# Optimization experiments

Measured on AMD Instinct MI355X. Metric: run time of the kernel, lower is better.

Reference implementation:

```python
import jax, jax.numpy as jnp
import numpy as np

B, N, D_MAX_LEN, D_LENGTH, D_MODEL, N_CLASS = 16, 1024, 512, 256, 128, 10
SAMPLE_K = 140  # factor(20) * ceil(ln(1024)) = 20*7; also n_top u (L_Q == L_K)


def setup_inputs() -> dict:
    key = jax.random.key(0)
    ks = jax.random.split(key, 10)
    s = 0.02
    return {
        "input_embedding": jax.random.normal(ks[0], (B, N, D_MAX_LEN), jnp.float32),
        "index_sample": jax.random.randint(ks[1], (N, SAMPLE_K), 0, N),
        # weights stored [in, out] (transpose of torch Linear.weight)
        "W_lin": jax.random.normal(ks[2], (D_MAX_LEN, D_LENGTH), jnp.float32) * s,
        "b_lin": jnp.zeros((D_LENGTH,), jnp.float32),
        "W_q": jax.random.normal(ks[3], (D_LENGTH, D_MODEL), jnp.float32) * s,
        "W_k": jax.random.normal(ks[4], (D_LENGTH, D_MODEL), jnp.float32) * s,
        "W_v": jax.random.normal(ks[5], (D_LENGTH, D_MODEL), jnp.float32) * s,
        "W_add": jax.random.normal(ks[6], (D_LENGTH, D_MODEL), jnp.float32) * s,
        "b_add": jnp.zeros((D_MODEL,), jnp.float32),
        "W_final": jax.random.normal(ks[7], (D_MODEL * N, N_CLASS), jnp.float32) * s,
        "b_final": jnp.zeros((N_CLASS,), jnp.float32),
    }


def reference(input_embedding, index_sample, W_lin, b_lin, W_q, W_k, W_v,
              W_add, b_add, W_final, b_final):
    # self.linear: [B, N, d_max_len] -> [B, N, d_length]
    x = input_embedding @ W_lin + b_lin
    b, n, _ = x.shape
    # single head (h=1): [B, 1, L, D]
    Q = (x @ W_q)[:, None]
    K = (x @ W_k)[:, None]
    V = (x @ W_v)[:, None]
    d = Q.shape[-1]
    L_K = n
    n_top = index_sample.shape[1]  # u == sample_k here

    # _prob_QK: gather sampled keys per query row, score against Q
    Kg = K[:, :, index_sample, :]                      # [B,1,L_Q,S,D]
    QK_sample = jnp.einsum('bhld,bhlsd->bhls', Q, Kg)  # [B,1,L_Q,S]
    M = QK_sample.max(-1) - QK_sample.sum(-1) / L_K    # sparsity measure
    _, M_top = jax.lax.top_k(M, n_top)                 # [B,1,u]

    Qr = jnp.take_along_axis(Q, M_top[..., None], axis=2)       # [B,1,u,D]
    scores = jnp.einsum('bhud,bhkd->bhuk', Qr, K) / np.sqrt(d)  # [B,1,u,L_K]

    # _get_initial_context (mask_flag=False): mean of V broadcast over L_Q
    ctx = jnp.broadcast_to(V.mean(axis=2, keepdims=True), V.shape)  # [B,1,L_Q,D]

    # _update_context: scatter softmax(scores) @ V into selected rows
    attn = jax.nn.softmax(scores, axis=-1)
    upd = jnp.einsum('bhuk,bhkd->bhud', attn, V)  # [B,1,u,D]
    bidx = jnp.arange(b)[:, None, None]
    hidx = jnp.arange(1)[None, :, None]
    ctx = ctx.at[bidx, hidx, M_top].set(upd)

    ctx = ctx[:, 0]                    # H=1 -> [B,N,D]
    out = ctx + (x @ W_add + b_add)    # residual add (dropout: eval mode)
    out = out.reshape(b, -1) @ W_final + b_final  # [B, n_class]
    return out
```

## Files before the change

### kernel.cpp

```cpp
#include <hip/hip_runtime.h>

typedef __attribute__((ext_vector_type(8))) short short8;
typedef __attribute__((ext_vector_type(8))) unsigned short ushort8;
typedef __attribute__((ext_vector_type(4))) float f32x4;
typedef unsigned short u16;
typedef unsigned int u32;
typedef __attribute__((address_space(1))) const u32 gu32;
typedef __attribute__((address_space(3))) u32 lu32;

__device__ __forceinline__ u16 f2bf(float f){
  unsigned u = __float_as_uint(f);
  u += 0x7FFF + ((u >> 16) & 1);
  return (u16)(u >> 16);
}
__device__ __forceinline__ float bf2f(u16 h){ return __uint_as_float(((unsigned)h) << 16); }

#define BB   16
#define NN   1024
#define DML  512
#define DL   256
#define DM   128
#define NC   10
#define SK   140
#define KTOT (NN*DM)

__global__ void k_prep(const float* __restrict__ Wlin, const float* __restrict__ Wq,
                       const float* __restrict__ Wk, const float* __restrict__ Wv,
                       const float* __restrict__ Wadd,
                       u16* __restrict__ wlinT, u16* __restrict__ w4T,
                       const float* __restrict__ Wf, u16* __restrict__ wf2,
                       const int* __restrict__ idxs, u16* __restrict__ idxp){
  int blk = blockIdx.x, t = threadIdx.x;
  if (blk < 512){
    int id = blk*256 + t;
    {
      int j = id >> 9;
      int k = id & 511;
      wlinT[id] = f2bf(Wlin[k*DL + j]);
    }
    {
      int j = id >> 8;
      int k = id & 255;
      const float* src = (j < 128) ? Wq : (j < 256) ? Wk : (j < 384) ? Wv : Wadd;
      int jj = j & 127;
      w4T[id] = f2bf(src[k*DM + jj]);
    }
  } else if (blk < 1792){
    int i4 = (blk-512)*256 + t;
    float4 v = ((const float4*)Wf)[i4];
    ushort4 o; o.x=f2bf(v.x); o.y=f2bf(v.y); o.z=f2bf(v.z); o.w=f2bf(v.w);
    ((ushort4*)wf2)[i4] = o;
  } else {
    int id = (blk-1792)*256 + t;
    int l = id / 144;
    int s = id - l*144;
    idxp[id] = (s < SK) ? (u16)idxs[l*SK + s] : (u16)0xFFFF;
  }
}

__device__ __forceinline__ void stage2(const u16* __restrict__ A, const u16* __restrict__ B,
                                       int K, int m0, int n0, int kb,
                                       u16* sA, u16* sB, int tid, int wave){
  #pragma unroll
  for (int i = 0; i < 4; ++i){
    int ci  = i*256 + tid;
    int row = ci >> 3;
    int kc  = (ci & 7) ^ (row & 7);
    __builtin_amdgcn_global_load_lds((gu32*)(A + (long)(m0+row)*K + kb + kc*8),
                                     (lu32*)(sA + (i*256 + wave*64)*8), 16, 0, 0);
    __builtin_amdgcn_global_load_lds((gu32*)(B + (long)(n0+row)*K + kb + kc*8),
                                     (lu32*)(sB + (i*256 + wave*64)*8), 16, 0, 0);
  }
}
__device__ __forceinline__ void compute64(const u16* sA, const u16* sB,
                                          int lane, int wrow, int wcol, f32x4 acc[4][4]){
  #pragma unroll
  for (int kk = 0; kk < 2; ++kk){
    short8 af[4], bfr[4];
    int cb = kk*4 + (lane >> 4);
    #pragma unroll
    for (int m_=0; m_<4; ++m_){
      int row = wrow + m_*16 + (lane & 15);
      af[m_] = *(const short8*)&sA[row*64 + ((cb ^ (row & 7)) << 3)];
    }
    #pragma unroll
    for (int n_=0; n_<4; ++n_){
      int row = wcol + n_*16 + (lane & 15);
      bfr[n_] = *(const short8*)&sB[row*64 + ((cb ^ (row & 7)) << 3)];
    }
    #pragma unroll
    for (int m_=0; m_<4; ++m_)
      #pragma unroll
      for (int n_=0; n_<4; ++n_)
        acc[m_][n_] = __builtin_amdgcn_mfma_f32_16x16x32_bf16(af[m_], bfr[n_], acc[m_][n_], 0, 0, 0);
  }
}

__global__ __launch_bounds__(256) void k_gemm_x(const float* __restrict__ A, const u16* __restrict__ B,
                                                const float* __restrict__ bias, u16* __restrict__ out){
  __shared__ u16 smem[12288];
  u16* sA = smem;
  u16* sB = smem + 4096;
  const int tid  = threadIdx.x;
  const int lane = tid & 63;
  const int wave = tid >> 6;
  const int wrow = (wave >> 1) * 32;
  const int wcol = (wave & 1) * 64;
  int m0 = blockIdx.x*64, n0 = blockIdx.y*128;
  f32x4 acc[2][4];
  f32x4 z = {0.f,0.f,0.f,0.f};
  #pragma unroll
  for (int m_=0;m_<2;++m_) for (int n_=0;n_<4;++n_) acc[m_][n_] = z;

  f32x4 ra[4];
  short8 rb[4];
  const int arow = tid >> 2, aq = tid & 3;

  {
    const float* src = A + (long)(m0+arow)*DML + aq*16;
    ra[0] = ((const f32x4*)src)[0]; ra[1] = ((const f32x4*)src)[1];
    ra[2] = ((const f32x4*)src)[2]; ra[3] = ((const f32x4*)src)[3];
    #pragma unroll
    for (int i=0;i<4;++i){
      int ci = i*256 + tid, row = ci>>3, kc = ci&7;
      rb[i] = *(const short8*)(B + (long)(n0+row)*DML + kc*8);
    }
  }
  {
    short8 o0, o1;
    #pragma unroll
    for (int j=0;j<4;++j){ o0[j]=(short)f2bf(ra[0][j]); o0[4+j]=(short)f2bf(ra[1][j]);
                           o1[j]=(short)f2bf(ra[2][j]); o1[4+j]=(short)f2bf(ra[3][j]); }
    int kc0 = aq*2, kc1 = aq*2+1;
    *(short8*)&sA[arow*64 + ((kc0 ^ (arow&7))<<3)] = o0;
    *(short8*)&sA[arow*64 + ((kc1 ^ (arow&7))<<3)] = o1;
    #pragma unroll
    for (int i=0;i<4;++i){
      int ci = i*256 + tid, row = ci>>3, kc = ci&7;
      *(short8*)&sB[row*64 + ((kc ^ (row&7))<<3)] = rb[i];
    }
  }
  __syncthreads();

  for (int tt = 0; tt < 8; ++tt){
    if (tt < 7){
      int kb = (tt+1)*64;
      const float* src = A + (long)(m0+arow)*DML + kb + aq*16;
      ra[0] = ((const f32x4*)src)[0]; ra[1] = ((const f32x4*)src)[1];
      ra[2] = ((const f32x4*)src)[2]; ra[3] = ((const f32x4*)src)[3];
      #pragma unroll
      for (int i=0;i<4;++i){
        int ci = i*256 + tid, row = ci>>3, kc = ci&7;
        rb[i] = *(const short8*)(B + (long)(n0+row)*DML + kb + kc*8);
      }
    }
    #pragma unroll
    for (int kk = 0; kk < 2; ++kk){
      short8 af[2], bfr[4];
      int cb = kk*4 + (lane >> 4);
      #pragma unroll
      for (int m_=0; m_<2; ++m_){
        int row = wrow + m_*16 + (lane & 15);
        af[m_] = *(const short8*)&sA[row*64 + ((cb ^ (row & 7)) << 3)];
      }
      #pragma unroll
      for (int n_=0; n_<4; ++n_){
        int row = wcol + n_*16 + (lane & 15);
        bfr[n_] = *(const short8*)&sB[row*64 + ((cb ^ (row & 7)) << 3)];
      }
      #pragma unroll
      for (int m_=0; m_<2; ++m_)
        #pragma unroll
        for (int n_=0; n_<4; ++n_)
          acc[m_][n_] = __builtin_amdgcn_mfma_f32_16x16x32_bf16(af[m_], bfr[n_], acc[m_][n_], 0, 0, 0);
    }
    __syncthreads();
    if (tt < 7){
      short8 o0, o1;
      #pragma unroll
      for (int j=0;j<4;++j){ o0[j]=(short)f2bf(ra[0][j]); o0[4+j]=(short)f2bf(ra[1][j]);
                             o1[j]=(short)f2bf(ra[2][j]); o1[4+j]=(short)f2bf(ra[3][j]); }
      int kc0 = aq*2, kc1 = aq*2+1;
      *(short8*)&sA[arow*64 + ((kc0 ^ (arow&7))<<3)] = o0;
      *(short8*)&sA[arow*64 + ((kc1 ^ (arow&7))<<3)] = o1;
      #pragma unroll
      for (int i=0;i<4;++i){
        int ci = i*256 + tid, row = ci>>3, kc = ci&7;
        *(short8*)&sB[row*64 + ((kc ^ (row&7))<<3)] = rb[i];
      }
      __syncthreads();
    }
  }

  u16* sC = sB;
  #pragma unroll
  for (int m_=0;m_<2;++m_)
    #pragma unroll
    for (int n_=0;n_<4;++n_)
      #pragma unroll
      for (int rr=0;rr<4;++rr){
        int row = wrow + m_*16 + (lane>>4)*4 + rr;
        int col = wcol + n_*16 + (lane & 15);
        sC[row*128 + col] = f2bf(acc[m_][n_][rr] + bias[n0 + col]);
      }
  __syncthreads();
  #pragma unroll
  for (int i = 0; i < 4; ++i){
    int ci = i*256 + tid;
    int row = ci >> 4, c = ci & 15;
    *(short8*)(out + (long)(m0+row)*DL + n0 + c*8) = *(const short8*)&sC[row*128 + c*8];
  }
}

__global__ __launch_bounds__(256) void k_gemm_qkva(const u16* __restrict__ A, const u16* __restrict__ B,
                                                   const float* __restrict__ badd,
                                                   u16* __restrict__ oq, u16* __restrict__ ok,
                                                   u16* __restrict__ ov, u16* __restrict__ oa,
                                                   u16* __restrict__ vT){
  __shared__ u16 smem[17408];
  u16* sA = smem;
  u16* sB = smem + 8192;
  const int tid = threadIdx.x, lane = tid & 63, wave = tid >> 6;
  const int wrow = (wave>>1)*64, wcol = (wave&1)*64;
  f32x4 acc[4][4];
  f32x4 z = {0.f,0.f,0.f,0.f};
  #pragma unroll
  for (int m_=0;m_<4;++m_) for (int n_=0;n_<4;++n_) acc[m_][n_] = z;
  int m0 = blockIdx.x*128;
  int tn = blockIdx.y;
  int n0 = tn*128;

  #pragma unroll
  for (int t = 0; t < 4; ++t){
    stage2(A, B, DL, m0, n0, t*64, sA, sB, tid, wave);
    __syncthreads();
    compute64(sA, sB, lane, wrow, wcol, acc);
    __syncthreads();
  }

  u16* dst = (tn==0) ? oq : (tn==1) ? ok : (tn==2) ? ov : oa;
  u16* sC = smem;
  #pragma unroll
  for (int m_=0;m_<4;++m_)
    #pragma unroll
    for (int n_=0;n_<4;++n_)
      #pragma unroll
      for (int r=0;r<4;++r){
        int row = wrow + m_*16 + (lane>>4)*4 + r;
        int col = wcol + n_*16 + (lane & 15);
        float v = acc[m_][n_][r];
        if (tn == 3) v += badd[col];
        sC[row*136 + col] = f2bf(v);
      }
  __syncthreads();
  u16* db = dst + (long)m0*DM;
  #pragma unroll
  for (int i = 0; i < 8; ++i){
    int ci = i*256 + tid;
    int row = ci >> 4, c = ci & 15;
    *(short8*)(db + (long)row*DM + c*8) = *(const short8*)&sC[row*136 + c*8];
  }
  if (tn == 2){
    int b2 = m0 >> 10, l0 = m0 & 1023;
    u16* vtb = vT + (long)b2*KTOT + l0;
    #pragma unroll
    for (int i = 0; i < 8; ++i){
      int gi = i*256 + tid;
      int d = gi >> 4, mc = gi & 15;
      ushort8 o;
      #pragma unroll
      for (int j = 0; j < 8; ++j) o[j] = sC[(mc*8+j)*136 + d];
      *(ushort8*)(vtb + (long)d*NN + mc*8) = o;
    }
  }
}

__global__ __launch_bounds__(256) void k_gemm_s(const u16* __restrict__ Q, const u16* __restrict__ Km,
                                                u16* __restrict__ S, const u16* __restrict__ idxp,
                                                float* __restrict__ pmax, float* __restrict__ psum){
  __shared__ u16 smem[16384];
  u16* sA = smem;
  u16* sB = smem + 8192;
  const int tid = threadIdx.x, lane = tid & 63, wave = tid >> 6;
  const int wrow = (wave>>1)*64, wcol = (wave&1)*64;
  f32x4 acc[4][4];
  f32x4 z = {0.f,0.f,0.f,0.f};
  #pragma unroll
  for (int m_=0;m_<4;++m_) for (int n_=0;n_<4;++n_) acc[m_][n_] = z;
  int b = blockIdx.x, n0 = blockIdx.y*128, m0 = blockIdx.z*128;
  const u16* A = Q  + (long)b*NN*DM;
  const u16* B = Km + (long)b*NN*DM;

  stage2(A, B, DM, m0, n0, 0, sA, sB, tid, wave);
  __syncthreads();
  compute64(sA, sB, lane, wrow, wcol, acc);
  __syncthreads();
  stage2(A, B, DM, m0, n0, 64, sA, sB, tid, wave);
  __syncthreads();
  compute64(sA, sB, lane, wrow, wcol, acc);
  __syncthreads();

  u16* sS = smem;
  #pragma unroll
  for (int m_=0;m_<4;++m_)
    #pragma unroll
    for (int n_=0;n_<4;++n_)
      #pragma unroll
      for (int r=0;r<4;++r){
        int row = wrow + m_*16 + (lane>>4)*4 + r;
        int col = wcol + n_*16 + (lane & 15);
        sS[row*128 + col] = f2bf(acc[m_][n_][r]);
      }
  __syncthreads();

  u16* Sb = S + (long)b*NN*NN + (long)m0*NN + n0;
  #pragma unroll
  for (int i = 0; i < 8; ++i){
    int ci = i*256 + tid;
    int row = ci >> 4, c = ci & 15;
    *(short8*)(Sb + (long)row*NN + c*8) = *(const short8*)&sS[row*128 + c*8];
  }

  int l = tid >> 1, h = tid & 1;
  const u16* ip = idxp + (long)(m0+l)*144 + h*72;
  float mx = -1e30f, sm = 0.f;
  #pragma unroll
  for (int j = 0; j < 9; ++j){
    ushort8 v = *(const ushort8*)(ip + j*8);
    #pragma unroll
    for (int e = 0; e < 8; ++e){
      int d = (int)v[e] - n0;
      if ((unsigned)d < 128u){
        float s = bf2f(sS[l*128 + d]);
        mx = fmaxf(mx, s); sm += s;
      }
    }
  }
  float mo = __shfl_xor(mx, 1), so = __shfl_xor(sm, 1);
  mx = fmaxf(mx, mo); sm += so;
  if (h == 0){
    int o = (b*8 + blockIdx.y)*NN + m0 + l;
    pmax[o] = mx; psum[o] = sm;
  }
}

__global__ __launch_bounds__(256) void k_rankvm(const float* __restrict__ pmax, const float* __restrict__ psum,
                                                int* __restrict__ partial,
                                                const u16* __restrict__ V, float* __restrict__ vmean){
  int blk = blockIdx.x, t = threadIdx.x;
  if (blk < 256){
    __shared__ float Ml[1024];
    int b = blk >> 4, jc = blk & 15;
    #pragma unroll
    for (int r=0;r<4;++r){
      int i = t + r*256;
      float mx = -1e30f, sm = 0.f;
      #pragma unroll
      for (int nb=0;nb<8;++nb){
        mx = fmaxf(mx, pmax[(b*8+nb)*NN + i]);
        sm += psum[(b*8+nb)*NN + i];
      }
      Ml[i] = mx - sm * (1.0f/1024.0f);
    }
    __syncthreads();
    float mi[4];
    int cnt[4] = {0,0,0,0};
    #pragma unroll
    for (int r=0;r<4;++r) mi[r] = Ml[t + r*256];
    int j0 = jc*64;
    for (int j = 0; j < 64; ++j){
      float mj = Ml[j0 + j];
      int jg = j0 + j;
      #pragma unroll
      for (int r=0;r<4;++r){
        int i = t + r*256;
        cnt[r] += (mj > mi[r]) || (mj == mi[r] && jg < i);
      }
    }
    int* pb = partial + (b*16 + jc)*NN;
    #pragma unroll
    for (int r=0;r<4;++r) pb[t + r*256] = cnt[r];
  } else {
    __shared__ float red[16][128];
    int b = blk - 256;
    int d8 = t & 15, seg = t >> 4;
    const u16* Vb = V + (long)b*KTOT + seg*64*DM + d8*8;
    float acc[8] = {0,0,0,0,0,0,0,0};
    for (int l = 0; l < 64; ++l){
      short8 v = *(const short8*)(Vb + l*DM);
      #pragma unroll
      for (int j=0;j<8;++j) acc[j] += bf2f((u16)v[j]);
    }
    #pragma unroll
    for (int j=0;j<8;++j) red[seg][d8*8+j] = acc[j];
    __syncthreads();
    if (t < 128){
      float s = 0.f;
      #pragma unroll
      for (int g=0;g<16;++g) s += red[g][t];
      vmean[b*DM + t] = s * (1.0f/1024.0f);
    }
  }
}

__global__ __launch_bounds__(1024) void k_sel(const int* __restrict__ partial, int* __restrict__ mtop,
                                              int* __restrict__ selmap){
  int b = blockIdx.x, i = threadIdx.x;
  int cnt = 0;
  #pragma unroll
  for (int jc = 0; jc < 16; ++jc) cnt += partial[(b*16 + jc)*NN + i];
  selmap[b*NN + i] = (cnt < SK) ? cnt : -1;
  if (cnt < SK) mtop[b*SK + cnt] = i;
}

__global__ __launch_bounds__(256) void k_attn(const u16* __restrict__ S, const u16* __restrict__ vT,
                                              const int* __restrict__ mtop, float* __restrict__ upd){
  __shared__ u16 sPt[2][16*72];
  __shared__ u16 sVt[128*64];
  __shared__ int   sBrow[16];
  __shared__ float sMx[16];
  __shared__ float sSum[16];
  int b = blockIdx.x, u0 = blockIdx.y*16, t = threadIdx.x;
  int lane = t & 63, wave = t >> 6;
  const float inv = 0.08838834764831845f;

  if (t < 16){
    int u = u0 + t; if (u > SK-1) u = SK-1;
    sBrow[t] = mtop[b*SK + u];
  }
  __syncthreads();
  int row = t >> 4, c = t & 15;
  const u16* Srow = S + (long)b*NN*NN + (long)sBrow[row]*NN;

  float mx = -1e30f;
  #pragma unroll
  for (int j = 0; j < 8; ++j){
    ushort8 v = *(const ushort8*)(Srow + c*8 + j*128);
    #pragma unroll
    for (int e = 0; e < 8; ++e) mx = fmaxf(mx, bf2f((u16)v[e]));
  }
  #pragma unroll
  for (int o = 1; o < 16; o <<= 1) mx = fmaxf(mx, __shfl_xor(mx, o));
  if (c == 0) sMx[row] = mx;
  __syncthreads();
  float mxr = sMx[row] * inv;
  const u16* vTb = vT + (long)b*KTOT;

  f32x4 acc[2];
  f32x4 z = {0.f,0.f,0.f,0.f};
  acc[0] = z; acc[1] = z;
  float ps = 0.f;

  for (int ks = 0; ks < 16; ++ks){
    #pragma unroll
    for (int i = 0; i < 4; ++i){
      int ci = i*256 + t;
      int r2 = ci >> 3;
      int kc = (ci & 7) ^ (r2 & 7);
      __builtin_amdgcn_global_load_lds((gu32*)(vTb + (long)r2*NN + ks*64 + kc*8),
                                       (lu32*)(sVt + (i*256 + wave*64)*8), 16, 0, 0);
    }
    u16* sp = sPt[ks & 1];
    {
      ushort4 s4 = *(const ushort4*)(Srow + ks*64 + c*4);
      float e0 = __expf(bf2f(s4.x)*inv - mxr);
      float e1 = __expf(bf2f(s4.y)*inv - mxr);
      float e2 = __expf(bf2f(s4.z)*inv - mxr);
      float e3 = __expf(bf2f(s4.w)*inv - mxr);
      ps += e0+e1+e2+e3;
      ushort4 pw; pw.x=f2bf(e0); pw.y=f2bf(e1); pw.z=f2bf(e2); pw.w=f2bf(e3);
      *(ushort4*)&sp[row*72 + c*4] = pw;
    }
    __syncthreads();
    #pragma unroll
    for (int kk = 0; kk < 2; ++kk){
      int cb = kk*4 + (lane >> 4);
      short8 af = *(const short8*)&sp[(lane & 15)*72 + cb*8];
      #pragma unroll
      for (int n_ = 0; n_ < 2; ++n_){
        int r2 = wave*32 + n_*16 + (lane & 15);
        short8 bf_ = *(const short8*)&sVt[r2*64 + ((cb ^ (r2 & 7)) << 3)];
        acc[n_] = __builtin_amdgcn_mfma_f32_16x16x32_bf16(af, bf_, acc[n_], 0, 0, 0);
      }
    }
    __syncthreads();
  }

  #pragma unroll
  for (int o = 1; o < 16; o <<= 1) ps += __shfl_xor(ps, o);
  if (c == 0) sSum[row] = ps;
  __syncthreads();
  int r0 = (lane >> 4) * 4;
  float rz[4];
  #pragma unroll
  for (int r = 0; r < 4; ++r) rz[r] = 1.0f / sSum[r0 + r];
  #pragma unroll
  for (int n_ = 0; n_ < 2; ++n_){
    int col = wave*32 + n_*16 + (lane & 15);
    #pragma unroll
    for (int r = 0; r < 4; ++r){
      int urow = u0 + r0 + r;
      if (urow < SK)
        upd[((long)b*SK + urow)*DM + col] = acc[n_][r] * rz[r];
    }
  }
}

__global__ __launch_bounds__(256) void k_final(const float* __restrict__ upd, const float* __restrict__ vmean,
                                               const int* __restrict__ selmap,
                                               const u16* __restrict__ Aad,
                                               const u16* __restrict__ wf2, float* __restrict__ part){
  int b = blockIdx.x, ch = blockIdx.y, t = threadIdx.x;
  long base = (long)b * KTOT;
  int k0 = ch * 4096;
  float acc[NC] = {0.f};
  for (int k = k0 + t; k < k0 + 4096; k += 256){
    int l = k >> 7, d = k & 127;
    int sel = selmap[b*NN + l];
    float c = (sel >= 0) ? upd[((long)b*SK + sel)*DM + d] : vmean[b*DM + d];
    float v = c + bf2f(Aad[base + k]);
    const u32* w32 = (const u32*)(wf2 + (long)k*NC);
    #pragma unroll
    for (int cc = 0; cc < 5; ++cc){
      u32 w = w32[cc];
      acc[2*cc]   += v * bf2f((u16)(w & 0xFFFF));
      acc[2*cc+1] += v * bf2f((u16)(w >> 16));
    }
  }
  __shared__ float lred[40];
  int lane = t & 63, wave = t >> 6;
  #pragma unroll
  for (int c = 0; c < NC; ++c){
    float v = acc[c];
    #pragma unroll
    for (int o=32;o;o>>=1) v += __shfl_xor(v,o);
    if (lane == 0) lred[wave*NC + c] = v;
  }
  __syncthreads();
  if (t < NC) part[(b*32 + ch)*NC + t] = lred[t] + lred[NC+t] + lred[2*NC+t] + lred[3*NC+t];
}

__global__ void k_out(const float* __restrict__ part, const float* __restrict__ bfin, float* __restrict__ out){
  int t = threadIdx.x;
  if (t < BB*NC){
    int b = t / NC, c = t % NC;
    float s = bfin[c];
    #pragma unroll
    for (int ch = 0; ch < 32; ++ch) s += part[(b*32 + ch)*NC + c];
    out[t] = s;
  }
}

extern "C" void kernel_launch(void* const* d_in, const int* in_sizes, int n_in,
                              void* d_out, int out_size, void* d_ws, size_t ws_size,
                              hipStream_t stream){
  const float* emb  = (const float*)d_in[0];
  const int*   idxs = (const int*)  d_in[1];
  const float* Wlin = (const float*)d_in[2];
  const float* blin = (const float*)d_in[3];
  const float* Wq   = (const float*)d_in[4];
  const float* Wk   = (const float*)d_in[5];
  const float* Wv   = (const float*)d_in[6];
  const float* Wadd = (const float*)d_in[7];
  const float* badd = (const float*)d_in[8];
  const float* Wfin = (const float*)d_in[9];
  const float* bfin = (const float*)d_in[10];
  float* out = (float*)d_out;

  char* p = (char*)d_ws;
  auto alloc = [&](size_t bytes)->char*{ char* r = p; p += (bytes + 255) & ~(size_t)255; return r; };
  u16*   wlinT  = (u16*)  alloc((size_t)DL*DML*2);
  u16*   w4T    = (u16*)  alloc((size_t)4*DM*DL*2);
  u16*   x_bf   = (u16*)  alloc((size_t)BB*NN*DL*2);
  u16*   q_bf   = (u16*)  alloc((size_t)BB*NN*DM*2);
  u16*   k_bf   = (u16*)  alloc((size_t)BB*NN*DM*2);
  u16*   v_bf   = (u16*)  alloc((size_t)BB*NN*DM*2);
  u16*   a_bf   = (u16*)  alloc((size_t)BB*NN*DM*2);
  u16*   vT     = (u16*)  alloc((size_t)BB*KTOT*2);
  u16*   s_bf   = (u16*)  alloc((size_t)BB*NN*NN*2);
  u16*   idxp   = (u16*)  alloc((size_t)NN*144*2);
  float* pmax   = (float*)alloc((size_t)BB*8*NN*4);
  float* psum   = (float*)alloc((size_t)BB*8*NN*4);
  int*   rankp  = (int*)  alloc((size_t)BB*16*NN*4);
  int*   mtop   = (int*)  alloc((size_t)BB*SK*4);
  int*   selmap = (int*)  alloc((size_t)BB*NN*4);
  float* vmean  = (float*)alloc((size_t)BB*DM*4);
  float* upd    = (float*)alloc((size_t)BB*SK*DM*4);
  u16*   wf2    = (u16*)  alloc((size_t)KTOT*NC*2);
  float* part   = (float*)alloc((size_t)BB*32*NC*4);

  k_prep<<<dim3(2368), dim3(256), 0, stream>>>(Wlin, Wq, Wk, Wv, Wadd, wlinT, w4T, Wfin, wf2, idxs, idxp);
  k_gemm_x<<<dim3(256, 2), dim3(256), 0, stream>>>(emb, wlinT, blin, x_bf);
  k_gemm_qkva<<<dim3(128, 4), dim3(256), 0, stream>>>(x_bf, w4T, badd, q_bf, k_bf, v_bf, a_bf, vT);
  k_gemm_s<<<dim3(16, 8, 8), dim3(256), 0, stream>>>(q_bf, k_bf, s_bf, idxp, pmax, psum);
  k_rankvm<<<dim3(272), dim3(256), 0, stream>>>(pmax, psum, rankp, v_bf, vmean);
  k_sel<<<dim3(BB), dim3(1024), 0, stream>>>(rankp, mtop, selmap);
  k_attn<<<dim3(BB, 9), dim3(256), 0, stream>>>(s_bf, vT, mtop, upd);
  k_final<<<dim3(BB, 32), dim3(256), 0, stream>>>(upd, vmean, selmap, a_bf, wf2, part);
  k_out<<<dim3(1), dim3(256), 0, stream>>>(part, bfin, out);
}
```

Before: 97.50 us.

## Split k_attn key dimension across two blocks and combine partials in k_final

Adds a split-K dimension to the attention kernel: each of two blocks handles half the keys and writes unnormalized partial outputs and partial softmax sums. k_final adds the two partials and normalizes them with reciprocal sums held in shared memory. This doubles the attention grid from 144 to 288 blocks so more of the GPU's compute units have work. In exchange it writes twice the partial data and reads two arrays in k_final. The row max is still computed over the full row, so the partials combine exactly.

```diff
diff --git a/kernel.cpp b/kernel.cpp
--- a/kernel.cpp
+++ b/kernel.cpp
@@ -414,13 +414,14 @@
 }
 
 __global__ __launch_bounds__(256) void k_attn(const u16* __restrict__ S, const u16* __restrict__ vT,
-                                              const int* __restrict__ mtop, float* __restrict__ upd){
+                                              const int* __restrict__ mtop,
+                                              float* __restrict__ updp, float* __restrict__ zsum){
   __shared__ u16 sPt[2][16*72];
   __shared__ u16 sVt[128*64];
   __shared__ int   sBrow[16];
   __shared__ float sMx[16];
   __shared__ float sSum[16];
-  int b = blockIdx.x, u0 = blockIdx.y*16, t = threadIdx.x;
+  int b = blockIdx.x, u0 = blockIdx.y*16, ksp = blockIdx.z, t = threadIdx.x;
   int lane = t & 63, wave = t >> 6;
   const float inv = 0.08838834764831845f;
 
@@ -451,7 +452,7 @@
   acc[0] = z; acc[1] = z;
   float ps = 0.f;
 
-  for (int ks = 0; ks < 16; ++ks){
+  for (int ks = ksp*8; ks < ksp*8 + 8; ++ks){
     #pragma unroll
     for (int i = 0; i < 4; ++i){
       int ci = i*256 + t;
@@ -490,10 +491,12 @@
   for (int o = 1; o < 16; o <<= 1) ps += __shfl_xor(ps, o);
   if (c == 0) sSum[row] = ps;
   __syncthreads();
+  if (t < 16){
+    int urow = u0 + t;
+    if (urow < SK) zsum[(ksp*BB + b)*SK + urow] = sSum[t];
+  }
   int r0 = (lane >> 4) * 4;
-  float rz[4];
-  #pragma unroll
-  for (int r = 0; r < 4; ++r) rz[r] = 1.0f / sSum[r0 + r];
+  float* up = updp + (long)ksp*BB*SK*DM;
   #pragma unroll
   for (int n_ = 0; n_ < 2; ++n_){
     int col = wave*32 + n_*16 + (lane & 15);
@@ -501,23 +504,36 @@
     for (int r = 0; r < 4; ++r){
       int urow = u0 + r0 + r;
       if (urow < SK)
-        upd[((long)b*SK + urow)*DM + col] = acc[n_][r] * rz[r];
-    }
-  }
-}
-
-__global__ __launch_bounds__(256) void k_final(const float* __restrict__ upd, const float* __restrict__ vmean,
+        up[((long)b*SK + urow)*DM + col] = acc[n_][r];
+    }
+  }
+}
+
+__global__ __launch_bounds__(256) void k_final(const float* __restrict__ updp, const float* __restrict__ zsum,
+                                               const float* __restrict__ vmean,
                                                const int* __restrict__ selmap,
                                                const u16* __restrict__ Aad,
                                                const u16* __restrict__ wf2, float* __restrict__ part){
+  __shared__ float rzs[SK];
   int b = blockIdx.x, ch = blockIdx.y, t = threadIdx.x;
+  for (int i = t; i < SK; i += 256)
+    rzs[i] = 1.0f / (zsum[b*SK + i] + zsum[(BB + b)*SK + i]);
+  __syncthreads();
   long base = (long)b * KTOT;
+  const float* up0 = updp;
+  const float* up1 = updp + (long)BB*SK*DM;
   int k0 = ch * 4096;
   float acc[NC] = {0.f};
   for (int k = k0 + t; k < k0 + 4096; k += 256){
     int l = k >> 7, d = k & 127;
     int sel = selmap[b*NN + l];
-    float c = (sel >= 0) ? upd[((long)b*SK + sel)*DM + d] : vmean[b*DM + d];
+    float c;
+    if (sel >= 0){
+      long ui = ((long)b*SK + sel)*DM + d;
+      c = (up0[ui] + up1[ui]) * rzs[sel];
+    } else {
+      c = vmean[b*DM + d];
+    }
     float v = c + bf2f(Aad[base + k]);
     const u32* w32 = (const u32*)(wf2 + (long)k*NC);
     #pragma unroll
@@ -585,7 +601,8 @@
   int*   mtop   = (int*)  alloc((size_t)BB*SK*4);
   int*   selmap = (int*)  alloc((size_t)BB*NN*4);
   float* vmean  = (float*)alloc((size_t)BB*DM*4);
-  float* upd    = (float*)alloc((size_t)BB*SK*DM*4);
+  float* updp   = (float*)alloc((size_t)2*BB*SK*DM*4);
+  float* zsum   = (float*)alloc((size_t)2*BB*SK*4);
   u16*   wf2    = (u16*)  alloc((size_t)KTOT*NC*2);
   float* part   = (float*)alloc((size_t)BB*32*NC*4);
 
@@ -595,7 +612,7 @@
   k_gemm_s<<<dim3(16, 8, 8), dim3(256), 0, stream>>>(q_bf, k_bf, s_bf, idxp, pmax, psum);
   k_rankvm<<<dim3(272), dim3(256), 0, stream>>>(pmax, psum, rankp, v_bf, vmean);
   k_sel<<<dim3(BB), dim3(1024), 0, stream>>>(rankp, mtop, selmap);
-  k_attn<<<dim3(BB, 9), dim3(256), 0, stream>>>(s_bf, vT, mtop, upd);
-  k_final<<<dim3(BB, 32), dim3(256), 0, stream>>>(upd, vmean, selmap, a_bf, wf2, part);
+  k_attn<<<dim3(BB, 9, 2), dim3(256), 0, stream>>>(s_bf, vT, mtop, updp, zsum);
+  k_final<<<dim3(BB, 32), dim3(256), 0, stream>>>(updp, zsum, vmean, selmap, a_bf, wf2, part);
   k_out<<<dim3(1), dim3(256), 0, stream>>>(part, bfin, out);
 }
```

Measured after the change: 95.27 us (median of 2 runs). 2.3% less time.
